# Kernel optimization log

Hardware: AMD Instinct MI355X
Metric: run time of the kernel (lower is better)

The kernel has to match this reference:

```python
import jax, jax.numpy as jnp
import numpy as np

B, T, D, H, O, L = 32, 512, 512, 512, 2, 2


def setup_inputs() -> dict:
    key = jax.random.key(0)
    ks = jax.random.split(key, 8)
    s_in = 1.0 / np.sqrt(D + H)
    s_h = 1.0 / np.sqrt(H + H)
    x = jax.random.normal(ks[0], (B, T, D), dtype=jnp.float32)
    # Fused gate weights per layer: columns ordered [forget | input | candidate | output]
    W0 = jax.random.uniform(ks[1], (D + H, 4 * H), jnp.float32, -s_in, s_in)
    b0 = jax.random.uniform(ks[2], (4 * H,), jnp.float32, -s_in, s_in)
    W1 = jax.random.uniform(ks[3], (H + H, 4 * H), jnp.float32, -s_h, s_h)
    b1 = jax.random.uniform(ks[4], (4 * H,), jnp.float32, -s_h, s_h)
    s_r = 1.0 / np.sqrt(H)
    Wr = jax.random.uniform(ks[5], (H, O), jnp.float32, -s_r, s_r)
    br = jax.random.uniform(ks[6], (O,), jnp.float32, -s_r, s_r)
    return {"x": x, "W0": W0, "b0": b0, "W1": W1, "b1": b1, "Wr": Wr, "br": br}


def _lstm_cell(xt, h, c, W, b):
    # One fused GEMM for all 4 gates, then elementwise gate math.
    z = jnp.concatenate([xt, h], axis=1) @ W + b  # [B, 4H]
    f, i, g, o = jnp.split(z, 4, axis=1)
    new_c = c * jax.nn.sigmoid(f) + jnp.tanh(g) * jax.nn.sigmoid(i)
    # NB: original module applies tanh to the OLD cell state c (faithful to source).
    new_h = jax.nn.sigmoid(o) * jnp.tanh(c)
    return new_h, new_c


def reference(x, W0, b0, W1, b1, Wr, br):
    Bb = x.shape[0]
    zeros = jnp.zeros((Bb, H), dtype=x.dtype)

    def step(carry, xt):
        h1, c1, h2, c2 = carry
        nh1, nc1 = _lstm_cell(xt, h1, c1, W0, b0)
        nh2, nc2 = _lstm_cell(nh1, h2, c2, W1, b1)
        return (nh1, nc1, nh2, nc2), nh2

    _, ys = jax.lax.scan(step, (zeros, zeros, zeros, zeros), jnp.swapaxes(x, 0, 1))
    out = jnp.swapaxes(ys, 0, 1)  # [B, T, H]
    return out @ Wr + br  # [B, T, O]
```

## Files before the change

### kernel.cpp

```cpp
#include <hip/hip_runtime.h>
#include <hip/hip_bf16.h>
#include <stdint.h>

typedef unsigned short u16;
typedef unsigned int u32;
typedef unsigned long long u64;
typedef __attribute__((ext_vector_type(8))) short bf16x8;
typedef __attribute__((ext_vector_type(4))) float f32x4;
typedef __attribute__((ext_vector_type(4))) u32 u32x4;

#define TT 512
#define WPS ((size_t)2048 * 1024)
#define ZRS 8
#define HRS 16
#define HRS2 4

#define LD16C(dst, addr) asm volatile("global_load_dwordx4 %0, %1, off sc0 sc1" : "=v"(dst) : "v"(addr))
#define LD8C(dst, addr)  asm volatile("global_load_dwordx2 %0, %1, off sc0 sc1" : "=v"(dst) : "v"(addr))
#define LD4C(dst, addr)  asm volatile("global_load_dword %0, %1, off sc0 sc1"   : "=v"(dst) : "v"(addr))
#define ST4C(addr, v)    asm volatile("global_store_dword %0, %1, off sc0 sc1"  :: "v"(addr), "v"(v) : "memory")
#define ST8C(addr, v)    asm volatile("global_store_dwordx2 %0, %1, off sc0 sc1":: "v"(addr), "v"(v) : "memory")
#define ST16C(addr, v)   asm volatile("global_store_dwordx4 %0, %1, off sc0 sc1":: "v"(addr), "v"(v) : "memory")
#define VM0()            do { asm volatile("s_waitcnt vmcnt(0)" ::: "memory"); \
                              __builtin_amdgcn_sched_barrier(0); } while (0)

__device__ __forceinline__ u16 f2bf(float f) {
  u32 u = __builtin_bit_cast(u32, f);
  return (u16)((u + 0x7FFFu + ((u >> 16) & 1u)) >> 16);
}
__device__ __forceinline__ float bf2f(u16 h) {
  u32 u = ((u32)h) << 16;
  return __builtin_bit_cast(float, u);
}
__device__ __forceinline__ float sigm(float x) { return 1.0f / (1.0f + expf(-x)); }
__device__ __forceinline__ f32x4 mfma16(bf16x8 a, bf16x8 b, f32x4 c) {
  return __builtin_amdgcn_mfma_f32_16x16x32_bf16(a, b, c, 0, 0, 0);
}
__device__ __forceinline__ u32 cvtpk(float a, float b) {
  u32 r;
  asm volatile("v_cvt_pk_bf16_f32 %0, %1, %2" : "=v"(r) : "v"(a), "v"(b));
  return r;
}
__device__ __forceinline__ void mark_err(u32* err) {
  __hip_atomic_fetch_add(err, 1u, __ATOMIC_RELAXED, __HIP_MEMORY_SCOPE_AGENT);
}
__device__ __forceinline__ u64 pack3(float v, u32 tag) {
  u16 p0 = f2bf(v); float r1 = v - bf2f(p0);
  u16 p1 = f2bf(r1); u16 p2 = f2bf(r1 - bf2f(p1));
  return (u64)((u32)p0 | ((u32)p1 << 16)) | ((u64)((u32)p2 | (tag << 16)) << 32);
}
__device__ __forceinline__ float zval(u64 w) {
  return bf2f((u16)(w & 0xFFFFu)) + bf2f((u16)((w >> 16) & 0xFFFFu))
       + bf2f((u16)((w >> 32) & 0xFFFFu));
}

__device__ __forceinline__ void wait_slots(const u32* slots, int ln, u32 tgt,
                                           u32* lastv, int* bail, u32* err) {
  if (*bail) return;
  if (__ballot(*lastv < tgt) == 0ull) return;
  const u32* ptr = slots + (ln & 31);
  int n = 0;
  for (;;) {
    u32 v;
    LD4C(v, ptr);
    VM0();
    if (v > *lastv) *lastv = v;
    if (__ballot(*lastv < tgt) == 0ull) return;
    __builtin_amdgcn_s_sleep(2);
    if (++n > 400000) { *bail = 1; if (ln == 0) mark_err(err); return; }
  }
}

__device__ __forceinline__ void head_poll(const u64* ptr, u32 texp, u32* err) {
  int n = 0;
  for (;;) {
    u64 hw;
    LD8C(hw, ptr);
    VM0();
    if (__ballot((u32)(hw >> 48) != texp) == 0ull) return;
    __builtin_amdgcn_s_sleep(1);
    if (++n > 600000) { if ((threadIdx.x & 63) == 0) mark_err(err); return; }
  }
}

__global__ void prep_w(const float* __restrict__ W, u16* __restrict__ WT) {
  int i = blockIdx.x * 256 + threadIdx.x;
  if (i >= 2048 * 1024) return;
  int n = i >> 10, k = i & 1023;
  float v = W[(size_t)k * 2048 + n];
  u16 p0 = f2bf(v);  float r  = v - bf2f(p0);
  u16 p1 = f2bf(r);  float r2 = r - bf2f(p1);
  u16 p2 = f2bf(r2);
  size_t o = (size_t)n * 1024 + k;
  WT[o] = p0;
  WT[WPS + o] = p1;
  WT[2 * WPS + o] = p2;
}

template <int LAYER>
__device__ void chain(char* smem, int p, int bid,
                      const float* __restrict__ bias,
                      const u16* __restrict__ WT,
                      const u64* Zring, u64* hG,
                      const u32* progOther, u32* progSelf,
                      u16* h2hi, u32* err) {
  u16* wl = (u16*)smem;
  float* zl = (float*)(smem + 131072);
  const int tid = threadIdx.x;

#pragma unroll 1
  for (int it = 0; it < 32; ++it) {
    int id = it * 256 + tid;
    int pl = id >> 12, rem = id & 4095, rho = rem >> 6, m = rem & 63;
    int n = ((rho >> 4) << 9) + (bid << 4) + (rho & 15);
    u32x4 v = *(const u32x4*)(WT + (size_t)pl * WPS + (size_t)n * 1024 + 512 + m * 8);
    int dst = pl * 65536 + rho * 1024 + ((m << 4) ^ ((rho & 7) << 4));
    *(u32x4*)((char*)wl + dst) = v;
  }

  const int ln = tid & 63, kq = tid >> 6;
  const int fr = ln & 15, kg8 = (ln >> 4) << 3;
  const int row = tid >> 4, hc = tid & 15;
  float bsv[4];
#pragma unroll
  for (int g = 0; g < 4; ++g) bsv[g] = bias[(g << 9) + (bid << 4) + hc];
  const int ka = kq * 128 + kg8;
  const u16* w2base[4];
#pragma unroll
  for (int nt = 0; nt < 4; ++nt)
    w2base[nt] = WT + 2 * WPS + (size_t)((nt << 9) + (bid << 4) + fr) * 1024 + 512 + ka;
  const int hrm = (LAYER == 1) ? (HRS - 1) : (HRS2 - 1);
  const int pcol = ((ln >> 1) << 4) + ((ln & 1) << 9);

  float creg = 0.0f;
  u32 lastbp = 0;
  int bail = 0;
  __syncthreads();

#pragma unroll 1
  for (int t = 0; t < TT; ++t) {
    if (LAYER == 1 && kq == 0 && t >= HRS - 1)
      wait_slots(progOther, ln, (u32)(t - (HRS - 1)), &lastbp, &bail, err);

    const size_t soff = (size_t)(t & hrm) * 8192;
    const u64* hb = hG + soff + (size_t)fr * 512 + ka;
    const u64* zb = Zring + (size_t)(t & (ZRS - 1)) * (16 * 2048) + (size_t)row * 2048
                  + (bid << 4) + hc;
    const u32 texp = (u32)t, zexp = (u32)(t + 1);

    u64 zw[4];
#pragma unroll
    for (int g = 0; g < 4; ++g) LD8C(zw[g], zb + ((size_t)g << 9));

    head_poll(hG + soff + pcol, texp, err);

    u32x4 hv[4][4];
    int tries = 0;
    for (;;) {
#pragma unroll
      for (int kt = 0; kt < 4; ++kt)
#pragma unroll
        for (int j = 0; j < 4; ++j) LD16C(hv[kt][j], hb + kt * 32 + 2 * j);
      VM0();
      u32 bad = 0;
#pragma unroll
      for (int kt = 0; kt < 4; ++kt)
#pragma unroll
        for (int j = 0; j < 4; ++j)
          bad |= ((hv[kt][j].y >> 16) ^ texp) | ((hv[kt][j].w >> 16) ^ texp);
      if (__ballot(bad != 0) == 0ull) break;
      if (++tries > 500000) { if (ln == 0) mark_err(err); break; }
      __builtin_amdgcn_s_sleep(1);
    }

    f32x4 acc[4] = {{0.f,0.f,0.f,0.f},{0.f,0.f,0.f,0.f},{0.f,0.f,0.f,0.f},{0.f,0.f,0.f,0.f}};
#pragma unroll
    for (int kt = 0; kt < 4; ++kt) {
      u32 r0[4], r1[4], r2[4];
#pragma unroll
      for (int j = 0; j < 4; ++j) {
        u32 lo0 = hv[kt][j].x, hi0 = hv[kt][j].y, lo1 = hv[kt][j].z, hi1 = hv[kt][j].w;
        r0[j] = (lo0 & 0xFFFFu) | (lo1 << 16);
        r1[j] = (lo0 >> 16) | (lo1 & 0xFFFF0000u);
        r2[j] = (hi0 & 0xFFFFu) | (hi1 << 16);
      }
      bf16x8 a0 = __builtin_bit_cast(bf16x8, *(u32x4*)r0);
      bf16x8 a1 = __builtin_bit_cast(bf16x8, *(u32x4*)r1);
      bf16x8 a2 = __builtin_bit_cast(bf16x8, *(u32x4*)r2);
#pragma unroll
      for (int nt = 0; nt < 4; ++nt) {
        int rho = (nt << 4) + fr;
        int kb = ((ka + kt * 32) << 1) ^ ((rho & 7) << 4);
        bf16x8 w0 = *(const bf16x8*)((char*)wl + rho * 1024 + kb);
        bf16x8 w1 = *(const bf16x8*)((char*)wl + 65536 + rho * 1024 + kb);
        bf16x8 w2 = *(const bf16x8*)(w2base[nt] + kt * 32);
        acc[nt] = mfma16(a0, w0, acc[nt]);
        acc[nt] = mfma16(a1, w0, acc[nt]);
        acc[nt] = mfma16(a2, w0, acc[nt]);
        acc[nt] = mfma16(a0, w1, acc[nt]);
        acc[nt] = mfma16(a1, w1, acc[nt]);
        acc[nt] = mfma16(a0, w2, acc[nt]);
      }
    }
    const int r4 = (ln >> 4) << 2;
    if (kq < 2) {
#pragma unroll
      for (int nt = 0; nt < 4; ++nt)
#pragma unroll
        for (int r = 0; r < 4; ++r)
          zl[(kq * 16 + r4 + r) * 66 + (nt << 4) + fr] = acc[nt][r];
    }
    __syncthreads();
    if (kq >= 2) {
#pragma unroll
      for (int nt = 0; nt < 4; ++nt)
#pragma unroll
        for (int r = 0; r < 4; ++r)
          zl[((kq - 2) * 16 + r4 + r) * 66 + (nt << 4) + fr] += acc[nt][r];
    }
    __syncthreads();

    int ztries = 0;
    for (;;) {
      u32 zbad = 0;
#pragma unroll
      for (int g = 0; g < 4; ++g) zbad |= ((u32)(zw[g] >> 48) ^ zexp);
      if (__ballot(zbad != 0) == 0ull) break;
      __builtin_amdgcn_s_sleep(1);
#pragma unroll
      for (int g = 0; g < 4; ++g) LD8C(zw[g], zb + ((size_t)g << 9));
      VM0();
      if (++ztries > 500000) { if (ln == 0) mark_err(err); break; }
    }
    float z4[4];
#pragma unroll
    for (int g = 0; g < 4; ++g)
      z4[g] = zl[row * 66 + (g << 4) + hc] + zl[(16 + row) * 66 + (g << 4) + hc]
            + zval(zw[g]) + bsv[g];
    float sf = sigm(z4[0]);
    float si = sigm(z4[1]);
    float tg = tanhf(z4[2]);
    float sog = sigm(z4[3]);
    float hn = sog * tanhf(creg);
    creg = creg * sf + tg * si;
    u64 word = pack3(hn, (u32)(t + 1));
    size_t ho = (size_t)((t + 1) & hrm) * 8192 + (size_t)row * 512 + (bid << 4) + hc;
    ST8C(hG + ho, word);
    if (LAYER == 2)
      h2hi[(size_t)(t + 1) * 16384 + (size_t)(p * 16 + row) * 512 + (bid << 4) + hc] =
          (u16)(word & 0xFFFFu);
    __syncthreads();
    if (tid == 0) ST4C(progSelf + bid, (u32)(t + 1));
  }
}

__device__ void worker_z0(char* smem, int s, int q, const float* __restrict__ x,
                          const u16* __restrict__ W0T, u64* Z0R,
                          const u32* prog1, u32* err) {
  u16* wl0 = (u16*)smem;
  float* zl = (float*)(smem + 131072);
  const int tid = threadIdx.x;

#pragma unroll 1
  for (int it = 0; it < 32; ++it) {
    int id = it * 256 + tid;
    int pl = id >> 12, rem = id & 4095, rho = rem >> 6, m = rem & 63;
    u32x4 v = *(const u32x4*)(W0T + (size_t)pl * WPS + (size_t)(64 * s + rho) * 1024 + m * 8);
    int dst = pl * 65536 + rho * 1024 + ((m << 4) ^ ((rho & 7) << 4));
    *(u32x4*)((char*)wl0 + dst) = v;
  }

  const int ln = tid & 63, kq = tid >> 6;
  const int fr = ln & 15, kg8 = (ln >> 4) << 3;
  const int row = tid >> 4, c4 = (tid & 15) * 4;
  const int ka = kq * 128 + kg8;
  u32 lastbp[2] = {0, 0};
  int bail = 0;
  __syncthreads();

#pragma unroll 1
  for (int k = 0;; ++k) {
    int t = 2 * k + q;
    if (t > 511) break;
    int nz = (k < 3) ? 2 : 1;
#pragma unroll 1
    for (int e = 0; e < nz; ++e) {
      int tz = (e == 0 && k < 3) ? t : t + 6;
      if (tz > 511) continue;
#pragma unroll 1
      for (int p = 0; p < 2; ++p) {
        if (kq == 0 && tz >= ZRS)
          wait_slots(prog1 + p * 32, ln, (u32)(tz - ZRS + 1), &lastbp[p], &bail, err);
        const float* xb = x + (size_t)(p * 16 + fr) * TT * 512 + (size_t)tz * 512 + ka;
        f32x4 acc[4] = {{0.f,0.f,0.f,0.f},{0.f,0.f,0.f,0.f},{0.f,0.f,0.f,0.f},{0.f,0.f,0.f,0.f}};
#pragma unroll
        for (int kt = 0; kt < 4; ++kt) {
          f32x4 f0 = *(const f32x4*)(xb + kt * 32);
          f32x4 f1 = *(const f32x4*)(xb + kt * 32 + 4);
          u32 r0[4], r1[4], r2[4];
#pragma unroll
          for (int j = 0; j < 4; ++j) {
            float v0 = (j < 2) ? f0[j * 2] : f1[(j - 2) * 2];
            float v1 = (j < 2) ? f0[j * 2 + 1] : f1[(j - 2) * 2 + 1];
            u32 pk0 = cvtpk(v0, v1);
            float h0 = __builtin_bit_cast(float, pk0 << 16);
            float h1f = __builtin_bit_cast(float, pk0 & 0xFFFF0000u);
            float q0 = v0 - h0, q1 = v1 - h1f;
            u32 pk1 = cvtpk(q0, q1);
            float g0 = __builtin_bit_cast(float, pk1 << 16);
            float g1 = __builtin_bit_cast(float, pk1 & 0xFFFF0000u);
            u32 s0 = __builtin_bit_cast(u32, q0 - g0);
            u32 s1 = __builtin_bit_cast(u32, q1 - g1);
            r0[j] = pk0; r1[j] = pk1;
            r2[j] = (s0 >> 16) | (s1 & 0xFFFF0000u);
          }
          bf16x8 a0 = __builtin_bit_cast(bf16x8, *(u32x4*)r0);
          bf16x8 a1 = __builtin_bit_cast(bf16x8, *(u32x4*)r1);
          bf16x8 a2 = __builtin_bit_cast(bf16x8, *(u32x4*)r2);
#pragma unroll
          for (int nt = 0; nt < 4; ++nt) {
            int rho = (nt << 4) + fr;
            int kb = ((ka + kt * 32) << 1) ^ ((rho & 7) << 4);
            bf16x8 w0 = *(const bf16x8*)((char*)wl0 + rho * 1024 + kb);
            bf16x8 w1 = *(const bf16x8*)((char*)wl0 + 65536 + rho * 1024 + kb);
            bf16x8 w2 = *(const bf16x8*)(W0T + 2 * WPS + (size_t)(64 * s + rho) * 1024 + ka + kt * 32);
            acc[nt] = mfma16(a0, w0, acc[nt]);
            acc[nt] = mfma16(a1, w0, acc[nt]);
            acc[nt] = mfma16(a2, w0, acc[nt]);
            acc[nt] = mfma16(a0, w1, acc[nt]);
            acc[nt] = mfma16(a1, w1, acc[nt]);
            acc[nt] = mfma16(a0, w2, acc[nt]);
          }
        }
        const int r4 = (ln >> 4) << 2;
        if (kq < 2) {
#pragma unroll
          for (int nt = 0; nt < 4; ++nt)
#pragma unroll
            for (int r = 0; r < 4; ++r)
              zl[(kq * 16 + r4 + r) * 66 + (nt << 4) + fr] = acc[nt][r];
        }
        __syncthreads();
        if (kq >= 2) {
#pragma unroll
          for (int nt = 0; nt < 4; ++nt)
#pragma unroll
            for (int r = 0; r < 4; ++r)
              zl[((kq - 2) * 16 + r4 + r) * 66 + (nt << 4) + fr] += acc[nt][r];
        }
        __syncthreads();
        u64 wv[4];
#pragma unroll
        for (int i = 0; i < 4; ++i) {
          float v = zl[row * 66 + c4 + i] + zl[(16 + row) * 66 + c4 + i];
          wv[i] = pack3(v, (u32)(tz + 1));
        }
        u64* dst = Z0R + (size_t)p * ZRS * 16 * 2048 + (size_t)(tz & (ZRS - 1)) * (16 * 2048)
                 + (size_t)row * 2048 + 64 * s + c4;
        u32x4 stA = { (u32)wv[0], (u32)(wv[0] >> 32), (u32)wv[1], (u32)(wv[1] >> 32) };
        u32x4 stB = { (u32)wv[2], (u32)(wv[2] >> 32), (u32)wv[3], (u32)(wv[3] >> 32) };
        ST16C(dst, stA);
        ST16C(dst + 2, stB);
        __syncthreads();
      }
    }
  }
}

__device__ void worker_zc(char* smem, int s, int q,
                          const u16* __restrict__ W1T, const u64* h1G, u64* ZcR,
                          const u32* prog2, u32* err) {
  u16* wl1 = (u16*)smem;
  float* zl = (float*)(smem + 131072);
  const int tid = threadIdx.x;

#pragma unroll 1
  for (int it = 0; it < 32; ++it) {
    int id = it * 256 + tid;
    int pl = id >> 12, rem = id & 4095, rho = rem >> 6, m = rem & 63;
    u32x4 v = *(const u32x4*)(W1T + (size_t)pl * WPS + (size_t)(64 * s + rho) * 1024 + m * 8);
    int dst = pl * 65536 + rho * 1024 + ((m << 4) ^ ((rho & 7) << 4));
    *(u32x4*)((char*)wl1 + dst) = v;
  }

  const int ln = tid & 63, kq = tid >> 6;
  const int fr = ln & 15, kg8 = (ln >> 4) << 3;
  const int row = tid >> 4, c4 = (tid & 15) * 4;
  const int ka = kq * 128 + kg8;
  const int pcol = ((ln >> 1) << 4) + ((ln & 1) << 9);
  u32 last2[2] = {0, 0};
  int bail = 0;
  __syncthreads();

#pragma unroll 1
  for (int k = 0;; ++k) {
    int t = 2 * k + q;
    if (t > 511) break;
#pragma unroll 1
    for (int p = 0; p < 2; ++p) {
      if (kq == 0 && t >= ZRS)
        wait_slots(prog2 + p * 32, ln, (u32)(t - ZRS + 1), &last2[p], &bail, err);
      const size_t sb = (size_t)p * HRS * 8192 + (size_t)((t + 1) & (HRS - 1)) * 8192;
      const u64* hb = h1G + sb + (size_t)fr * 512 + ka;
      const u32 texp = (u32)(t + 1);
      head_poll(h1G + sb + pcol, texp, err);
      u32x4 hv[4][4];
      int tries = 0;
      for (;;) {
#pragma unroll
        for (int kt = 0; kt < 4; ++kt)
#pragma unroll
          for (int j = 0; j < 4; ++j) LD16C(hv[kt][j], hb + kt * 32 + 2 * j);
        VM0();
        u32 bad = 0;
#pragma unroll
        for (int kt = 0; kt < 4; ++kt)
#pragma unroll
          for (int j = 0; j < 4; ++j)
            bad |= ((hv[kt][j].y >> 16) ^ texp) | ((hv[kt][j].w >> 16) ^ texp);
        if (__ballot(bad != 0) == 0ull) break;
        if (++tries > 500000) { if (ln == 0) mark_err(err); break; }
        __builtin_amdgcn_s_sleep(1);
      }
      f32x4 acc[4] = {{0.f,0.f,0.f,0.f},{0.f,0.f,0.f,0.f},{0.f,0.f,0.f,0.f},{0.f,0.f,0.f,0.f}};
#pragma unroll
      for (int kt = 0; kt < 4; ++kt) {
        u32 r0[4], r1[4], r2[4];
#pragma unroll
        for (int j = 0; j < 4; ++j) {
          u32 lo0 = hv[kt][j].x, hi0 = hv[kt][j].y, lo1 = hv[kt][j].z, hi1 = hv[kt][j].w;
          r0[j] = (lo0 & 0xFFFFu) | (lo1 << 16);
          r1[j] = (lo0 >> 16) | (lo1 & 0xFFFF0000u);
          r2[j] = (hi0 & 0xFFFFu) | (hi1 << 16);
        }
        bf16x8 a0 = __builtin_bit_cast(bf16x8, *(u32x4*)r0);
        bf16x8 a1 = __builtin_bit_cast(bf16x8, *(u32x4*)r1);
        bf16x8 a2 = __builtin_bit_cast(bf16x8, *(u32x4*)r2);
#pragma unroll
        for (int nt = 0; nt < 4; ++nt) {
          int rho = (nt << 4) + fr;
          int kb = ((ka + kt * 32) << 1) ^ ((rho & 7) << 4);
          bf16x8 w0 = *(const bf16x8*)((char*)wl1 + rho * 1024 + kb);
          bf16x8 w1 = *(const bf16x8*)((char*)wl1 + 65536 + rho * 1024 + kb);
          bf16x8 w2 = *(const bf16x8*)(W1T + 2 * WPS + (size_t)(64 * s + rho) * 1024 + ka + kt * 32);
          acc[nt] = mfma16(a0, w0, acc[nt]);
          acc[nt] = mfma16(a1, w0, acc[nt]);
          acc[nt] = mfma16(a2, w0, acc[nt]);
          acc[nt] = mfma16(a0, w1, acc[nt]);
          acc[nt] = mfma16(a1, w1, acc[nt]);
          acc[nt] = mfma16(a0, w2, acc[nt]);
        }
      }
      const int r4 = (ln >> 4) << 2;
      if (kq < 2) {
#pragma unroll
        for (int nt = 0; nt < 4; ++nt)
#pragma unroll
          for (int r = 0; r < 4; ++r)
            zl[(kq * 16 + r4 + r) * 66 + (nt << 4) + fr] = acc[nt][r];
      }
      __syncthreads();
      if (kq >= 2) {
#pragma unroll
        for (int nt = 0; nt < 4; ++nt)
#pragma unroll
          for (int r = 0; r < 4; ++r)
            zl[((kq - 2) * 16 + r4 + r) * 66 + (nt << 4) + fr] += acc[nt][r];
      }
      __syncthreads();
      u64 wv[4];
#pragma unroll
      for (int i = 0; i < 4; ++i) {
        float v = zl[row * 66 + c4 + i] + zl[(16 + row) * 66 + c4 + i];
        wv[i] = pack3(v, (u32)(t + 1));
      }
      u64* dst = ZcR + (size_t)p * ZRS * 16 * 2048 + (size_t)(t & (ZRS - 1)) * (16 * 2048)
               + (size_t)row * 2048 + 64 * s + c4;
      u32x4 stA = { (u32)wv[0], (u32)(wv[0] >> 32), (u32)wv[1], (u32)(wv[1] >> 32) };
      u32x4 stB = { (u32)wv[2], (u32)(wv[2] >> 32), (u32)wv[3], (u32)(wv[3] >> 32) };
      ST16C(dst, stA);
      ST16C(dst + 2, stB);
      __syncthreads();
    }
  }
}

__global__ void __launch_bounds__(256, 1) mega(
    const float* __restrict__ x,
    const float* __restrict__ bias0, const float* __restrict__ bias1,
    const u16* __restrict__ W0T, const u16* __restrict__ W1T,
    u64* Z0R, u64* ZcR, u64* h1G, u64* h2G, u16* h2hi, u32* flags) {
  __shared__ char smem[139520];
  const int blk = blockIdx.x;
  const int r8 = blk & 7, g8 = blk >> 3;
  u32* prog1 = flags;
  u32* prog2 = flags + 64;
  u32* err = flags + 128;
  if (r8 < 2) {
    int p = r8;
    chain<1>(smem, p, g8, bias0, W0T,
             Z0R + (size_t)p * ZRS * 16 * 2048, h1G + (size_t)p * HRS * 8192,
             prog2 + p * 32, prog1 + p * 32, nullptr, err);
  } else if (r8 < 4) {
    int p = r8 - 2;
    chain<2>(smem, p, g8, bias1, W1T,
             ZcR + (size_t)p * ZRS * 16 * 2048, h2G + (size_t)p * HRS2 * 8192,
             nullptr, prog2 + p * 32, h2hi, err);
  } else if (r8 < 6) {
    worker_zc(smem, g8, r8 - 4, W1T, h1G, ZcR, prog2, err);
  } else {
    worker_z0(smem, g8, r8 - 6, x, W0T, Z0R, prog1, err);
  }
}

__global__ void proj(const u16* __restrict__ y,
                     const float* __restrict__ Wr, const float* __restrict__ br,
                     float* __restrict__ out) {
  int gw = (blockIdx.x * blockDim.x + threadIdx.x) >> 6;
  int ln = threadIdx.x & 63;
  int t = gw >> 5, b = gw & 31;
  const u16* yp = y + (size_t)(t + 1) * 16384 + (size_t)b * 512 + ln * 8;
  u32x4 v = *(const u32x4*)yp;
  float p0 = 0.f, p1 = 0.f;
#pragma unroll
  for (int jj = 0; jj < 8; ++jj) {
    u16 hh = (u16)((v[jj >> 1] >> ((jj & 1) * 16)) & 0xFFFFu);
    float yv = bf2f(hh);
    int j = ln * 8 + jj;
    p0 += yv * Wr[j * 2 + 0];
    p1 += yv * Wr[j * 2 + 1];
  }
#pragma unroll
  for (int o = 32; o; o >>= 1) { p0 += __shfl_down(p0, o, 64); p1 += __shfl_down(p1, o, 64); }
  if (ln == 0) {
    out[((size_t)b * 512 + t) * 2 + 0] = p0 + br[0];
    out[((size_t)b * 512 + t) * 2 + 1] = p1 + br[1];
  }
}

__global__ void fail_mark(float* out, float code) {
  if (threadIdx.x == 0 && blockIdx.x == 0) out[0] = code;
}
__global__ void err_check(const u32* flags, float* out) {
  if (threadIdx.x == 0 && blockIdx.x == 0) {
    u32 e = flags[128];
    if (e) out[0] = 1.0e6f + (float)e;
  }
}

extern "C" void kernel_launch(void* const* d_in, const int* in_sizes, int n_in,
                              void* d_out, int out_size, void* d_ws, size_t ws_size,
                              hipStream_t stream) {
  (void)in_sizes; (void)n_in; (void)out_size;
  const float* x  = (const float*)d_in[0];
  const float* W0 = (const float*)d_in[1];
  const float* b0 = (const float*)d_in[2];
  const float* W1 = (const float*)d_in[3];
  const float* b1 = (const float*)d_in[4];
  const float* Wr = (const float*)d_in[5];
  const float* br = (const float*)d_in[6];
  float* out = (float*)d_out;

  char* ws = (char*)d_ws;
  size_t off = 0;
  auto take = [&](size_t n) { char* p = ws + off; off = (off + n + 255) & ~(size_t)255; return p; };

  u16* W0T  = (u16*)take(3 * WPS * 2);
  u16* W1T  = (u16*)take(3 * WPS * 2);
  u64* Z0R  = (u64*)take((size_t)2 * ZRS * 16 * 2048 * 8);
  u64* ZcR  = (u64*)take((size_t)2 * ZRS * 16 * 2048 * 8);
  u64* h1G  = (u64*)take((size_t)2 * HRS * 8192 * 8);
  u64* h2G  = (u64*)take((size_t)2 * HRS2 * 8192 * 8);
  u16* h2hi = (u16*)take((size_t)513 * 16384 * 2);
  u32* flags = (u32*)take(129 * 4);

  if (off > ws_size) {
    fail_mark<<<1, 1, 0, stream>>>(out, 2.0e6f);
    return;
  }

  (void)hipMemsetAsync(flags, 0, 129 * 4, stream);
  (void)hipMemsetAsync(Z0R, 0, (size_t)2 * ZRS * 16 * 2048 * 8, stream);
  (void)hipMemsetAsync(ZcR, 0, (size_t)2 * ZRS * 16 * 2048 * 8, stream);
  (void)hipMemsetAsync(h1G, 0, (size_t)2 * HRS * 8192 * 8, stream);
  (void)hipMemsetAsync(h2G, 0, (size_t)2 * HRS2 * 8192 * 8, stream);

  prep_w<<<8192, 256, 0, stream>>>(W0, W0T);
  prep_w<<<8192, 256, 0, stream>>>(W1, W1T);
  (void)hipGetLastError();
  mega<<<256, 256, 0, stream>>>(x, b0, b1, W0T, W1T,
                                Z0R, ZcR, h1G, h2G, h2hi, flags);
  if (hipGetLastError() != hipSuccess) {
    fail_mark<<<1, 1, 0, stream>>>(out, 3.0e6f);
    return;
  }
  proj<<<4096, 256, 0, stream>>>(h2hi, Wr, br, out);
  err_check<<<1, 1, 0, stream>>>(flags, out);
}
```

Before: 3.542 ms.

## Load h optimistically before polling and deepen Z0 and h2 rings

In the layer chains and the Zc worker, the full h tile is now loaded and checked for the expected timestep tag first. The head_poll spin and retry loop run only when that check fails, which saves a polling round trip when data is already present. Separately, the Z0 ring grows to 16 slots and the worker_z0 prefetch lead doubles, and the h2 ring grows to 8 slots, so producers can run further ahead of consumers. The cost is more ring memory and wasted loads when the optimistic read comes too early.

```diff
diff --git a/kernel.cpp b/kernel.cpp
--- a/kernel.cpp
+++ b/kernel.cpp
@@ -11,9 +11,10 @@
 
 #define TT 512
 #define WPS ((size_t)2048 * 1024)
-#define ZRS 8
+#define ZRS0 16
+#define ZRSC 8
 #define HRS 16
-#define HRS2 4
+#define HRS2 8
 
 #define LD16C(dst, addr) asm volatile("global_load_dwordx4 %0, %1, off sc0 sc1" : "=v"(dst) : "v"(addr))
 #define LD8C(dst, addr)  asm volatile("global_load_dwordx2 %0, %1, off sc0 sc1" : "=v"(dst) : "v"(addr))
@@ -97,7 +98,7 @@
   WT[2 * WPS + o] = p2;
 }
 
-template <int LAYER>
+template <int LAYER, int ZR>
 __device__ void chain(char* smem, int p, int bid,
                       const float* __restrict__ bias,
                       const u16* __restrict__ WT,
@@ -144,33 +145,47 @@
 
     const size_t soff = (size_t)(t & hrm) * 8192;
     const u64* hb = hG + soff + (size_t)fr * 512 + ka;
-    const u64* zb = Zring + (size_t)(t & (ZRS - 1)) * (16 * 2048) + (size_t)row * 2048
+    const u64* zb = Zring + (size_t)(t & (ZR - 1)) * (16 * 2048) + (size_t)row * 2048
                   + (bid << 4) + hc;
     const u32 texp = (u32)t, zexp = (u32)(t + 1);
 
     u64 zw[4];
 #pragma unroll
     for (int g = 0; g < 4; ++g) LD8C(zw[g], zb + ((size_t)g << 9));
-
-    head_poll(hG + soff + pcol, texp, err);
-
     u32x4 hv[4][4];
-    int tries = 0;
-    for (;;) {
-#pragma unroll
-      for (int kt = 0; kt < 4; ++kt)
-#pragma unroll
-        for (int j = 0; j < 4; ++j) LD16C(hv[kt][j], hb + kt * 32 + 2 * j);
-      VM0();
+#pragma unroll
+    for (int kt = 0; kt < 4; ++kt)
+#pragma unroll
+      for (int j = 0; j < 4; ++j) LD16C(hv[kt][j], hb + kt * 32 + 2 * j);
+    VM0();
+
+    {
       u32 bad = 0;
 #pragma unroll
       for (int kt = 0; kt < 4; ++kt)
 #pragma unroll
         for (int j = 0; j < 4; ++j)
           bad |= ((hv[kt][j].y >> 16) ^ texp) | ((hv[kt][j].w >> 16) ^ texp);
-      if (__ballot(bad != 0) == 0ull) break;
-      if (++tries > 500000) { if (ln == 0) mark_err(err); break; }
-      __builtin_amdgcn_s_sleep(1);
+      if (__ballot(bad != 0) != 0ull) {
+        head_poll(hG + soff + pcol, texp, err);
+        int tries = 0;
+        for (;;) {
+#pragma unroll
+          for (int kt = 0; kt < 4; ++kt)
+#pragma unroll
+            for (int j = 0; j < 4; ++j) LD16C(hv[kt][j], hb + kt * 32 + 2 * j);
+          VM0();
+          u32 bad2 = 0;
+#pragma unroll
+          for (int kt = 0; kt < 4; ++kt)
+#pragma unroll
+            for (int j = 0; j < 4; ++j)
+              bad2 |= ((hv[kt][j].y >> 16) ^ texp) | ((hv[kt][j].w >> 16) ^ texp);
+          if (__ballot(bad2 != 0) == 0ull) break;
+          if (++tries > 500000) { if (ln == 0) mark_err(err); break; }
+          __builtin_amdgcn_s_sleep(1);
+        }
+      }
     }
 
     f32x4 acc[4] = {{0.f,0.f,0.f,0.f},{0.f,0.f,0.f,0.f},{0.f,0.f,0.f,0.f},{0.f,0.f,0.f,0.f}};
@@ -282,15 +297,15 @@
   for (int k = 0;; ++k) {
     int t = 2 * k + q;
     if (t > 511) break;
-    int nz = (k < 3) ? 2 : 1;
+    int nz = (k < 6) ? 2 : 1;
 #pragma unroll 1
     for (int e = 0; e < nz; ++e) {
-      int tz = (e == 0 && k < 3) ? t : t + 6;
+      int tz = (e == 0 && k < 6) ? t : t + 12;
       if (tz > 511) continue;
 #pragma unroll 1
       for (int p = 0; p < 2; ++p) {
-        if (kq == 0 && tz >= ZRS)
-          wait_slots(prog1 + p * 32, ln, (u32)(tz - ZRS + 1), &lastbp[p], &bail, err);
+        if (kq == 0 && tz >= ZRS0)
+          wait_slots(prog1 + p * 32, ln, (u32)(tz - ZRS0 + 1), &lastbp[p], &bail, err);
         const float* xb = x + (size_t)(p * 16 + fr) * TT * 512 + (size_t)tz * 512 + ka;
         f32x4 acc[4] = {{0.f,0.f,0.f,0.f},{0.f,0.f,0.f,0.f},{0.f,0.f,0.f,0.f},{0.f,0.f,0.f,0.f}};
 #pragma unroll
@@ -355,7 +370,7 @@
           float v = zl[row * 66 + c4 + i] + zl[(16 + row) * 66 + c4 + i];
           wv[i] = pack3(v, (u32)(tz + 1));
         }
-        u64* dst = Z0R + (size_t)p * ZRS * 16 * 2048 + (size_t)(tz & (ZRS - 1)) * (16 * 2048)
+        u64* dst = Z0R + (size_t)p * ZRS0 * 16 * 2048 + (size_t)(tz & (ZRS0 - 1)) * (16 * 2048)
                  + (size_t)row * 2048 + 64 * s + c4;
         u32x4 stA = { (u32)wv[0], (u32)(wv[0] >> 32), (u32)wv[1], (u32)(wv[1] >> 32) };
         u32x4 stB = { (u32)wv[2], (u32)(wv[2] >> 32), (u32)wv[3], (u32)(wv[3] >> 32) };
@@ -398,30 +413,47 @@
     if (t > 511) break;
 #pragma unroll 1
     for (int p = 0; p < 2; ++p) {
-      if (kq == 0 && t >= ZRS)
-        wait_slots(prog2 + p * 32, ln, (u32)(t - ZRS + 1), &last2[p], &bail, err);
+      if (kq == 0 && t >= ZRSC)
+        wait_slots(prog2 + p * 32, ln, (u32)(t - ZRSC + 1), &last2[p], &bail, err);
       const size_t sb = (size_t)p * HRS * 8192 + (size_t)((t + 1) & (HRS - 1)) * 8192;
       const u64* hb = h1G + sb + (size_t)fr * 512 + ka;
       const u32 texp = (u32)(t + 1);
-      head_poll(h1G + sb + pcol, texp, err);
+
       u32x4 hv[4][4];
-      int tries = 0;
-      for (;;) {
-#pragma unroll
-        for (int kt = 0; kt < 4; ++kt)
-#pragma unroll
-          for (int j = 0; j < 4; ++j) LD16C(hv[kt][j], hb + kt * 32 + 2 * j);
-        VM0();
+#pragma unroll
+      for (int kt = 0; kt < 4; ++kt)
+#pragma unroll
+        for (int j = 0; j < 4; ++j) LD16C(hv[kt][j], hb + kt * 32 + 2 * j);
+      VM0();
+      {
         u32 bad = 0;
 #pragma unroll
         for (int kt = 0; kt < 4; ++kt)
 #pragma unroll
           for (int j = 0; j < 4; ++j)
             bad |= ((hv[kt][j].y >> 16) ^ texp) | ((hv[kt][j].w >> 16) ^ texp);
-        if (__ballot(bad != 0) == 0ull) break;
-        if (++tries > 500000) { if (ln == 0) mark_err(err); break; }
-        __builtin_amdgcn_s_sleep(1);
-      }
+        if (__ballot(bad != 0) != 0ull) {
+          head_poll(h1G + sb + pcol, texp, err);
+          int tries = 0;
+          for (;;) {
+#pragma unroll
+            for (int kt = 0; kt < 4; ++kt)
+#pragma unroll
+              for (int j = 0; j < 4; ++j) LD16C(hv[kt][j], hb + kt * 32 + 2 * j);
+            VM0();
+            u32 bad2 = 0;
+#pragma unroll
+            for (int kt = 0; kt < 4; ++kt)
+#pragma unroll
+              for (int j = 0; j < 4; ++j)
+                bad2 |= ((hv[kt][j].y >> 16) ^ texp) | ((hv[kt][j].w >> 16) ^ texp);
+            if (__ballot(bad2 != 0) == 0ull) break;
+            if (++tries > 500000) { if (ln == 0) mark_err(err); break; }
+            __builtin_amdgcn_s_sleep(1);
+          }
+        }
+      }
+
       f32x4 acc[4] = {{0.f,0.f,0.f,0.f},{0.f,0.f,0.f,0.f},{0.f,0.f,0.f,0.f},{0.f,0.f,0.f,0.f}};
 #pragma unroll
       for (int kt = 0; kt < 4; ++kt) {
@@ -474,7 +506,7 @@
         float v = zl[row * 66 + c4 + i] + zl[(16 + row) * 66 + c4 + i];
         wv[i] = pack3(v, (u32)(t + 1));
       }
-      u64* dst = ZcR + (size_t)p * ZRS * 16 * 2048 + (size_t)(t & (ZRS - 1)) * (16 * 2048)
+      u64* dst = ZcR + (size_t)p * ZRSC * 16 * 2048 + (size_t)(t & (ZRSC - 1)) * (16 * 2048)
                + (size_t)row * 2048 + 64 * s + c4;
       u32x4 stA = { (u32)wv[0], (u32)(wv[0] >> 32), (u32)wv[1], (u32)(wv[1] >> 32) };
       u32x4 stB = { (u32)wv[2], (u32)(wv[2] >> 32), (u32)wv[3], (u32)(wv[3] >> 32) };
@@ -498,14 +530,14 @@
   u32* err = flags + 128;
   if (r8 < 2) {
     int p = r8;
-    chain<1>(smem, p, g8, bias0, W0T,
-             Z0R + (size_t)p * ZRS * 16 * 2048, h1G + (size_t)p * HRS * 8192,
-             prog2 + p * 32, prog1 + p * 32, nullptr, err);
+    chain<1, ZRS0>(smem, p, g8, bias0, W0T,
+                   Z0R + (size_t)p * ZRS0 * 16 * 2048, h1G + (size_t)p * HRS * 8192,
+                   prog2 + p * 32, prog1 + p * 32, nullptr, err);
   } else if (r8 < 4) {
     int p = r8 - 2;
-    chain<2>(smem, p, g8, bias1, W1T,
-             ZcR + (size_t)p * ZRS * 16 * 2048, h2G + (size_t)p * HRS2 * 8192,
-             nullptr, prog2 + p * 32, h2hi, err);
+    chain<2, ZRSC>(smem, p, g8, bias1, W1T,
+                   ZcR + (size_t)p * ZRSC * 16 * 2048, h2G + (size_t)p * HRS2 * 8192,
+                   nullptr, prog2 + p * 32, h2hi, err);
   } else if (r8 < 6) {
     worker_zc(smem, g8, r8 - 4, W1T, h1G, ZcR, prog2, err);
   } else {
@@ -567,8 +599,8 @@
 
   u16* W0T  = (u16*)take(3 * WPS * 2);
   u16* W1T  = (u16*)take(3 * WPS * 2);
-  u64* Z0R  = (u64*)take((size_t)2 * ZRS * 16 * 2048 * 8);
-  u64* ZcR  = (u64*)take((size_t)2 * ZRS * 16 * 2048 * 8);
+  u64* Z0R  = (u64*)take((size_t)2 * ZRS0 * 16 * 2048 * 8);
+  u64* ZcR  = (u64*)take((size_t)2 * ZRSC * 16 * 2048 * 8);
   u64* h1G  = (u64*)take((size_t)2 * HRS * 8192 * 8);
   u64* h2G  = (u64*)take((size_t)2 * HRS2 * 8192 * 8);
   u16* h2hi = (u16*)take((size_t)513 * 16384 * 2);
@@ -580,8 +612,8 @@
   }
 
   (void)hipMemsetAsync(flags, 0, 129 * 4, stream);
-  (void)hipMemsetAsync(Z0R, 0, (size_t)2 * ZRS * 16 * 2048 * 8, stream);
-  (void)hipMemsetAsync(ZcR, 0, (size_t)2 * ZRS * 16 * 2048 * 8, stream);
+  (void)hipMemsetAsync(Z0R, 0, (size_t)2 * ZRS0 * 16 * 2048 * 8, stream);
+  (void)hipMemsetAsync(ZcR, 0, (size_t)2 * ZRSC * 16 * 2048 * 8, stream);
   (void)hipMemsetAsync(h1G, 0, (size_t)2 * HRS * 8192 * 8, stream);
   (void)hipMemsetAsync(h2G, 0, (size_t)2 * HRS2 * 8192 * 8, stream);
 
```

Result: slower. 4.072 ms (+14.9%).
